# Performance work log

Hardware: AMD Instinct MI355X
Metric: run time of the kernel (lower is better)

The kernel has to match this reference:

```python
import jax, jax.numpy as jnp
import numpy as np

N_NODES = 100000      # total nodes across batch (50 graphs x 2000 nodes)
N_EDGES = 1600000     # avg degree 16
D = 64                # input_dim = hidden dims = output_dim
L = 3                 # number of GIN layers actually executed
NUM_GRAPHS = 50
NODES_PER_GRAPH = 2000
CAT_D = L * D         # 192, concat of hidden layer outputs


def setup_inputs() -> dict:
    key = jax.random.key(0)
    ks = jax.random.split(key, 12)
    s = 1.0 / np.sqrt(D)          # torch Linear init scale
    s2 = 1.0 / np.sqrt(CAT_D)
    return {
        "x": jax.random.normal(ks[0], (N_NODES, D), jnp.float32),
        "edge_index": jax.random.randint(ks[1], (2, N_EDGES), 0, N_NODES),
        "edge_weight": jax.random.uniform(ks[2], (N_EDGES,), jnp.float32),
        "batch": jnp.repeat(jnp.arange(NUM_GRAPHS), NODES_PER_GRAPH),  # sorted graph ids
        "W1": jax.random.uniform(ks[3], (L, D, D), jnp.float32, -s, s),
        "b1": jax.random.uniform(ks[4], (L, D), jnp.float32, -s, s),
        "W2": jax.random.uniform(ks[5], (L, D, D), jnp.float32, -s, s),
        "b2": jax.random.uniform(ks[6], (L, D), jnp.float32, -s, s),
        "eps": jnp.zeros((L,), jnp.float32),  # train_eps init 0.0
        "lin_w": jax.random.uniform(ks[7], (CAT_D, D), jnp.float32, -s2, s2),
        "lin_b": jax.random.uniform(ks[8], (D,), jnp.float32, -s2, s2),
    }


def reference(x, edge_index, edge_weight, batch, W1, b1, W2, b2, eps, lin_w, lin_b):
    src, dst = edge_index[0], edge_index[1]
    ew = edge_weight[:, None]
    h = x
    hiddens = []
    for l in range(L):
        # weighted GIN: aggregate sum_j w_ij * h_j at destination nodes
        agg = jax.ops.segment_sum(h[src] * ew, dst, num_segments=N_NODES)
        z = (1.0 + eps[l]) * h + agg
        # GIN MLP: Linear -> LeakyReLU -> Linear
        z = jax.nn.leaky_relu(z @ W1[l] + b1[l]) @ W2[l] + b2[l]
        hiddens.append(z)              # hiddens store pre-activation conv output
        h = jax.nn.leaky_relu(z)       # activation feeds next layer (dropout=0)
    h_cat = jnp.concatenate(hiddens, axis=-1)          # [N, 192]
    pooled = jax.ops.segment_sum(h_cat, batch, num_segments=NUM_GRAPHS)  # global_add_pool
    return pooled @ lin_w + lin_b                      # [NUM_GRAPHS, D]
```

## Files before the change

### kernel.cpp

```cpp
#include <hip/hip_runtime.h>

#define N_NODES 100000
#define N_EDGES 1600000
#define DD 64
#define NLAYER 3
#define NUM_GRAPHS 50
#define NODES_PER_GRAPH 2000
#define CAT_D (NLAYER * DD)
#define MROWS 80
#define MLP_THREADS 320
#define LPITCH 72

#define NPB 256
#define NB ((N_NODES + NPB - 1) / NPB)
#define BPAD 6144
#define ECHUNK 4096

#define GNODES 32
#define WECAP 288

typedef __attribute__((ext_vector_type(8))) short short8;
typedef __attribute__((ext_vector_type(4))) float float4v;

__device__ __forceinline__ float bf2f(unsigned short u) {
    return __uint_as_float(((unsigned)u) << 16);
}
__device__ __forceinline__ unsigned short f2bf(float f) {
    unsigned u = __float_as_uint(f);
    unsigned r = u + 0x7FFF + ((u >> 16) & 1);
    return (unsigned short)(r >> 16);
}
__device__ __forceinline__ float bflo(unsigned u) {
    return __uint_as_float(u << 16);
}
__device__ __forceinline__ float bfhi(unsigned u) {
    return __uint_as_float(u & 0xFFFF0000u);
}

__global__ __launch_bounds__(256) void convert_x_kernel(
    const float* __restrict__ x, unsigned short* __restrict__ hx)
{
    int i = (blockIdx.x * blockDim.x + threadIdx.x) * 4;
    if (i + 3 < N_NODES * DD) {
        float4 v = *(const float4*)&x[i];
        hx[i]     = f2bf(v.x);
        hx[i + 1] = f2bf(v.y);
        hx[i + 2] = f2bf(v.z);
        hx[i + 3] = f2bf(v.w);
    }
}

__global__ __launch_bounds__(256) void convert_w_kernel(
    const float* __restrict__ W1, const float* __restrict__ W2,
    unsigned short* __restrict__ W1t, unsigned short* __restrict__ W2t,
    int* __restrict__ cursor)
{
    int idx = blockIdx.x * blockDim.x + threadIdx.x;
    if (idx < NB) cursor[idx] = idx * BPAD;
    if (idx >= 2 * NLAYER * DD * DD) return;
    int which = idx / (NLAYER * DD * DD);
    int rem = idx % (NLAYER * DD * DD);
    int l = rem / (DD * DD);
    int t = rem % (DD * DD);
    int n = t >> 6, k = t & 63;
    const float* W = which ? W2 : W1;
    unsigned short* Wt = which ? W2t : W1t;
    Wt[l * DD * DD + n * DD + k] = f2bf(W[l * DD * DD + k * DD + n]);
}

__global__ __launch_bounds__(256) void bin_kernel(
    const int* __restrict__ src, const int* __restrict__ dst,
    const float* __restrict__ ew, int* __restrict__ cursor,
    uint2* __restrict__ binned)
{
    __shared__ uint2 stage[ECHUNK];
    __shared__ unsigned short bkt[ECHUNK];
    __shared__ int cnt[512];
    __shared__ int base[512];
    __shared__ int ssum[256];
    __shared__ int gbase[512];

    const int tid = threadIdx.x;
    const int start = blockIdx.x * ECHUNK;
    const int count = min(ECHUNK, N_EDGES - start);

    cnt[tid] = 0;
    cnt[tid + 256] = 0;
    __syncthreads();

    unsigned pk1[16], pk2[16];
    int eb[16], er[16];
    #pragma unroll
    for (int k = 0; k < 16; ++k) {
        int i = tid + k * 256;
        if (i < count) {
            int e = start + i;
            int s = src[e];
            int d = dst[e];
            float w = ew[e];
            int b = d >> 8;
            pk1[k] = (unsigned)s | ((unsigned)(d & 255) << 17);
            pk2[k] = __float_as_uint(w);
            eb[k] = b;
            er[k] = atomicAdd(&cnt[b], 1);
        } else {
            eb[k] = -1;
        }
    }
    __syncthreads();

    int c0 = cnt[2 * tid], c1 = cnt[2 * tid + 1];
    ssum[tid] = c0 + c1;
    __syncthreads();
    for (int off = 1; off < 256; off <<= 1) {
        int x = (tid >= off) ? ssum[tid - off] : 0;
        __syncthreads();
        ssum[tid] += x;
        __syncthreads();
    }
    int ex = (tid > 0) ? ssum[tid - 1] : 0;
    base[2 * tid] = ex;
    base[2 * tid + 1] = ex + c0;

    if (2 * tid < NB && c0 > 0)     gbase[2 * tid]     = atomicAdd(&cursor[2 * tid], c0);
    if (2 * tid + 1 < NB && c1 > 0) gbase[2 * tid + 1] = atomicAdd(&cursor[2 * tid + 1], c1);
    __syncthreads();

    #pragma unroll
    for (int k = 0; k < 16; ++k) {
        if (eb[k] >= 0) {
            int p = base[eb[k]] + er[k];
            stage[p].x = pk1[k];
            stage[p].y = pk2[k];
            bkt[p] = (unsigned short)eb[k];
        }
    }
    __syncthreads();

    for (int i = tid; i < count; i += 256) {
        int b = bkt[i];
        binned[gbase[b] + (i - base[b])] = stage[i];
    }
}

__global__ __launch_bounds__(256) void localsort_kernel(
    const int* __restrict__ cursor, const uint2* __restrict__ binned,
    uint2* __restrict__ s_edge, int* __restrict__ beg, int* __restrict__ end)
{
    __shared__ int deg[NPB];
    __shared__ int rb[NPB];
    __shared__ int cur[NPB];

    const int nb = blockIdx.x;
    const int tid = threadIdx.x;
    const int bstart = nb * BPAD;
    const int count = cursor[nb] - bstart;

    deg[tid] = 0;
    __syncthreads();
    for (int i = tid; i < count; i += 256) {
        unsigned w = binned[bstart + i].x;
        atomicAdd(&deg[(w >> 17) & 255], 1);
    }
    __syncthreads();

    int v = deg[tid];
    rb[tid] = v;
    __syncthreads();
    for (int off = 1; off < 256; off <<= 1) {
        int x = (tid >= off) ? rb[tid - off] : 0;
        __syncthreads();
        rb[tid] += x;
        __syncthreads();
    }
    int ex = rb[tid] - v;
    cur[tid] = ex;
    int node = nb * NPB + tid;
    if (node < N_NODES) {
        beg[node] = bstart + ex;
        end[node] = bstart + ex + v;
    }
    __syncthreads();

    for (int i = tid; i < count; i += 256) {
        uint2 e = binned[bstart + i];
        int d = (e.x >> 17) & 255;
        int r = atomicAdd(&cur[d], 1);
        uint2 o;
        o.x = e.x & 0x1FFFF;
        o.y = e.y;
        s_edge[bstart + r] = o;
    }
}

__global__ __launch_bounds__(256) void gather_kernel(
    const uint4* __restrict__ h4, const int* __restrict__ beg,
    const int* __restrict__ end, const uint2* __restrict__ s_edge,
    const float* __restrict__ eps, int l, uint4* __restrict__ z4)
{
    __shared__ uint2 eds[4 * WECAP];

    const int w    = threadIdx.x >> 6;
    const int lane = threadIdx.x & 63;
    const int o    = lane >> 3;
    const int fl   = lane & 7;
    const int nbase = blockIdx.x * GNODES + w * 8;
    const int node  = nbase + o;

    const int ebeg = beg[nbase];
    const int cnt  = end[nbase + 7] - ebeg;
    uint2* wl = &eds[w * WECAP];
    const bool lds_ok = (cnt <= WECAP);
    if (lds_ok) {
        for (int i = lane; i < cnt; i += 64) wl[i] = s_edge[ebeg + i];
    }

    const int gbeg = beg[node];
    const int deg  = end[node] - gbeg;

    float acc[4][8];
    #pragma unroll
    for (int c = 0; c < 4; ++c)
        #pragma unroll
        for (int j = 0; j < 8; ++j) acc[c][j] = 0.f;

    const uint4* hfl = h4 + fl;

    if (lds_ok) {
        const int bi = gbeg - ebeg;
        for (int it = 0; it < deg; it += 4) {
            #pragma unroll
            for (int c = 0; c < 4; ++c) {
                bool ok = (it + c) < deg;
                int idx = ok ? (bi + it + c) : bi;
                uint2 p = wl[idx];
                float wv = ok ? __uint_as_float(p.y) : 0.f;
                uint4 r = hfl[(long)p.x * 8];
                acc[c][0] += bflo(r.x) * wv;  acc[c][1] += bfhi(r.x) * wv;
                acc[c][2] += bflo(r.y) * wv;  acc[c][3] += bfhi(r.y) * wv;
                acc[c][4] += bflo(r.z) * wv;  acc[c][5] += bfhi(r.z) * wv;
                acc[c][6] += bflo(r.w) * wv;  acc[c][7] += bfhi(r.w) * wv;
            }
        }
    } else {
        for (int it = 0; it < deg; it += 4) {
            #pragma unroll
            for (int c = 0; c < 4; ++c) {
                bool ok = (it + c) < deg;
                int idx = ok ? (gbeg + it + c) : gbeg;
                uint2 p = s_edge[idx];
                float wv = ok ? __uint_as_float(p.y) : 0.f;
                uint4 r = hfl[(long)p.x * 8];
                acc[c][0] += bflo(r.x) * wv;  acc[c][1] += bfhi(r.x) * wv;
                acc[c][2] += bflo(r.y) * wv;  acc[c][3] += bfhi(r.y) * wv;
                acc[c][4] += bflo(r.z) * wv;  acc[c][5] += bfhi(r.z) * wv;
                acc[c][6] += bflo(r.w) * wv;  acc[c][7] += bfhi(r.w) * wv;
            }
        }
    }

    float s[8];
    #pragma unroll
    for (int j = 0; j < 8; ++j)
        s[j] = (acc[0][j] + acc[1][j]) + (acc[2][j] + acc[3][j]);

    const float e1 = 1.0f + eps[l];
    uint4 selfr = hfl[(long)node * 8];
    float z0 = e1 * bflo(selfr.x) + s[0];
    float z1 = e1 * bfhi(selfr.x) + s[1];
    float z2 = e1 * bflo(selfr.y) + s[2];
    float z3 = e1 * bfhi(selfr.y) + s[3];
    float z4v = e1 * bflo(selfr.z) + s[4];
    float z5 = e1 * bfhi(selfr.z) + s[5];
    float z6 = e1 * bflo(selfr.w) + s[6];
    float z7 = e1 * bfhi(selfr.w) + s[7];
    uint4 ov;
    ov.x = (unsigned)f2bf(z0) | ((unsigned)f2bf(z1) << 16);
    ov.y = (unsigned)f2bf(z2) | ((unsigned)f2bf(z3) << 16);
    ov.z = (unsigned)f2bf(z4v) | ((unsigned)f2bf(z5) << 16);
    ov.w = (unsigned)f2bf(z6) | ((unsigned)f2bf(z7) << 16);
    z4[(long)node * 8 + fl] = ov;
}

__global__ __launch_bounds__(MLP_THREADS) void mlp_kernel(
    const unsigned short* __restrict__ z_in,
    const unsigned short* __restrict__ W1t, const unsigned short* __restrict__ W2t,
    const float* __restrict__ b1l, const float* __restrict__ b2l,
    int l, unsigned short* __restrict__ h_out, float* __restrict__ pooled)
{
    __shared__ __align__(16) unsigned short zs[MROWS * LPITCH];
    __shared__ __align__(16) unsigned short w1s[DD * LPITCH];
    __shared__ __align__(16) unsigned short w2s[DD * LPITCH];
    __shared__ float red[5 * DD];

    const int tid  = threadIdx.x;
    const int lane = tid & 63;
    const int w    = tid >> 6;
    const int m15  = lane & 15;
    const int quad = lane >> 4;
    const long base = (long)blockIdx.x * MROWS;

    for (int idx = tid; idx < MROWS * 8; idx += MLP_THREADS) {
        int row = idx >> 3, seg = idx & 7;
        *(int4*)&zs[row * LPITCH + seg * 8] =
            *(const int4*)&z_in[(base + row) * DD + seg * 8];
    }
    for (int idx = tid; idx < DD * 8; idx += MLP_THREADS) {
        int row = idx >> 3, seg = idx & 7;
        *(int4*)&w1s[row * LPITCH + seg * 8] =
            *(const int4*)&W1t[(size_t)l * DD * DD + row * DD + seg * 8];
        *(int4*)&w2s[row * LPITCH + seg * 8] =
            *(const int4*)&W2t[(size_t)l * DD * DD + row * DD + seg * 8];
    }
    __syncthreads();

    {
        short8 a0 = *(const short8*)&zs[(w * 16 + m15) * LPITCH + quad * 8];
        short8 a1 = *(const short8*)&zs[(w * 16 + m15) * LPITCH + 32 + quad * 8];
        #pragma unroll
        for (int n = 0; n < 4; ++n) {
            short8 b0 = *(const short8*)&w1s[(n * 16 + m15) * LPITCH + quad * 8];
            short8 b1 = *(const short8*)&w1s[(n * 16 + m15) * LPITCH + 32 + quad * 8];
            float4v acc = {0.f, 0.f, 0.f, 0.f};
            acc = __builtin_amdgcn_mfma_f32_16x16x32_bf16(a0, b0, acc, 0, 0, 0);
            acc = __builtin_amdgcn_mfma_f32_16x16x32_bf16(a1, b1, acc, 0, 0, 0);
            int col = n * 16 + m15;
            float bv = b1l[col];
            #pragma unroll
            for (int r = 0; r < 4; ++r) {
                int row = w * 16 + quad * 4 + r;
                float t = acc[r] + bv;
                t = t > 0.0f ? t : 0.01f * t;
                zs[row * LPITCH + col] = f2bf(t);
            }
        }
    }

    float psum[4];
    {
        short8 a0 = *(const short8*)&zs[(w * 16 + m15) * LPITCH + quad * 8];
        short8 a1 = *(const short8*)&zs[(w * 16 + m15) * LPITCH + 32 + quad * 8];
        #pragma unroll
        for (int n = 0; n < 4; ++n) {
            short8 b0 = *(const short8*)&w2s[(n * 16 + m15) * LPITCH + quad * 8];
            short8 b1 = *(const short8*)&w2s[(n * 16 + m15) * LPITCH + 32 + quad * 8];
            float4v acc = {0.f, 0.f, 0.f, 0.f};
            acc = __builtin_amdgcn_mfma_f32_16x16x32_bf16(a0, b0, acc, 0, 0, 0);
            acc = __builtin_amdgcn_mfma_f32_16x16x32_bf16(a1, b1, acc, 0, 0, 0);
            int col = n * 16 + m15;
            float bv = b2l[col];
            float ps = 0.0f;
            #pragma unroll
            for (int r = 0; r < 4; ++r) {
                int row = w * 16 + quad * 4 + r;
                float z2 = acc[r] + bv;
                ps += z2;
                float hv = z2 > 0.0f ? z2 : 0.01f * z2;
                zs[row * LPITCH + col] = f2bf(hv);
            }
            psum[n] = ps;
        }
    }
    #pragma unroll
    for (int n = 0; n < 4; ++n) {
        float v = psum[n];
        v += __shfl_xor(v, 16);
        v += __shfl_xor(v, 32);
        if (quad == 0) red[w * DD + n * 16 + m15] = v;
    }
    __syncthreads();

    for (int idx = tid; idx < MROWS * 8; idx += MLP_THREADS) {
        int row = idx >> 3, seg = idx & 7;
        *(int4*)&h_out[(base + row) * DD + seg * 8] =
            *(const int4*)&zs[row * LPITCH + seg * 8];
    }
    if (tid < DD) {
        float tot = red[tid] + red[DD + tid] + red[2 * DD + tid]
                  + red[3 * DD + tid] + red[4 * DD + tid];
        int g = blockIdx.x / (NODES_PER_GRAPH / MROWS);
        atomicAdd(&pooled[g * CAT_D + l * DD + tid], tot);
    }
}

__global__ __launch_bounds__(64) void final_kernel(
    const float* __restrict__ pooled, const float* __restrict__ lin_w,
    const float* __restrict__ lin_b, float* __restrict__ out)
{
    int g = blockIdx.x;
    int j = threadIdx.x;
    float acc = lin_b[j];
    for (int k = 0; k < CAT_D; ++k)
        acc += pooled[g * CAT_D + k] * lin_w[k * DD + j];
    out[g * DD + j] = acc;
}

extern "C" void kernel_launch(void* const* d_in, const int* in_sizes, int n_in,
                              void* d_out, int out_size, void* d_ws, size_t ws_size,
                              hipStream_t stream)
{
    const float* x     = (const float*)d_in[0];
    const int*   ei    = (const int*)d_in[1];
    const float* ew    = (const float*)d_in[2];
    const float* W1    = (const float*)d_in[4];
    const float* b1    = (const float*)d_in[5];
    const float* W2    = (const float*)d_in[6];
    const float* b2    = (const float*)d_in[7];
    const float* eps   = (const float*)d_in[8];
    const float* lin_w = (const float*)d_in[9];
    const float* lin_b = (const float*)d_in[10];
    float* out = (float*)d_out;

    const int* src = ei;
    const int* dst = ei + N_EDGES;

    char* wsb = (char*)d_ws;
    size_t off = 0;
    auto alloc = [&](size_t bytes) -> void* {
        off = (off + 15) & ~(size_t)15;
        void* p = wsb + off;
        off += bytes;
        return p;
    };
    unsigned short* hX   = (unsigned short*)alloc((size_t)N_NODES * DD * 2);
    unsigned short* hA   = (unsigned short*)alloc((size_t)N_NODES * DD * 2);
    unsigned short* zbuf = (unsigned short*)alloc((size_t)N_NODES * DD * 2);
    unsigned short* W1t  = (unsigned short*)alloc((size_t)NLAYER * DD * DD * 2);
    unsigned short* W2t  = (unsigned short*)alloc((size_t)NLAYER * DD * DD * 2);
    float* pooled        = (float*)alloc((size_t)NUM_GRAPHS * CAT_D * 4);
    int*   cursor        = (int*)alloc((size_t)NB * 4);
    int*   beg           = (int*)alloc((size_t)N_NODES * 4);
    int*   end_          = (int*)alloc((size_t)N_NODES * 4);
    uint2* binned        = (uint2*)alloc((size_t)NB * BPAD * 8);
    uint2* s_edge        = (uint2*)alloc((size_t)NB * BPAD * 8);

    convert_x_kernel<<<(N_NODES * DD / 4 + 255) / 256, 256, 0, stream>>>(x, hX);
    convert_w_kernel<<<(2 * NLAYER * DD * DD + 255) / 256, 256, 0, stream>>>(
        W1, W2, W1t, W2t, cursor);

    bin_kernel<<<(N_EDGES + ECHUNK - 1) / ECHUNK, 256, 0, stream>>>(
        src, dst, ew, cursor, binned);
    localsort_kernel<<<NB, 256, 0, stream>>>(cursor, binned, s_edge, beg, end_);

    hipMemsetAsync(pooled, 0, NUM_GRAPHS * CAT_D * sizeof(float), stream);

    const unsigned short* h_cur = hX;
    unsigned short* h_nexts[3] = { hA, hX, hA };
    for (int l = 0; l < NLAYER; ++l) {
        gather_kernel<<<N_NODES / GNODES, 256, 0, stream>>>(
            (const uint4*)h_cur, beg, end_, s_edge, eps, l,
            (uint4*)zbuf);

        unsigned short* h_next = h_nexts[l];
        mlp_kernel<<<N_NODES / MROWS, MLP_THREADS, 0, stream>>>(
            zbuf, W1t, W2t,
            b1 + (size_t)l * DD, b2 + (size_t)l * DD,
            l, h_next, pooled);
        h_cur = h_next;
    }

    final_kernel<<<NUM_GRAPHS, 64, 0, stream>>>(pooled, lin_w, lin_b, out);
}
```

Before: 280.0 us.

## Fuse neighbor gather into MLP kernel and skip final layer hidden write

```diff
diff --git a/kernel.cpp b/kernel.cpp
--- a/kernel.cpp
+++ b/kernel.cpp
@@ -16,15 +16,11 @@
 #define BPAD 6144
 #define ECHUNK 4096
 
-#define GNODES 32
 #define WECAP 288
 
 typedef __attribute__((ext_vector_type(8))) short short8;
 typedef __attribute__((ext_vector_type(4))) float float4v;
 
-__device__ __forceinline__ float bf2f(unsigned short u) {
-    return __uint_as_float(((unsigned)u) << 16);
-}
 __device__ __forceinline__ unsigned short f2bf(float f) {
     unsigned u = __float_as_uint(f);
     unsigned r = u + 0x7FFF + ((u >> 16) & 1);
@@ -193,118 +189,25 @@
     }
 }
 
-__global__ __launch_bounds__(256) void gather_kernel(
+__global__ __launch_bounds__(MLP_THREADS) void layer_kernel(
     const uint4* __restrict__ h4, const int* __restrict__ beg,
     const int* __restrict__ end, const uint2* __restrict__ s_edge,
-    const float* __restrict__ eps, int l, uint4* __restrict__ z4)
-{
-    __shared__ uint2 eds[4 * WECAP];
-
-    const int w    = threadIdx.x >> 6;
-    const int lane = threadIdx.x & 63;
-    const int o    = lane >> 3;
-    const int fl   = lane & 7;
-    const int nbase = blockIdx.x * GNODES + w * 8;
-    const int node  = nbase + o;
-
-    const int ebeg = beg[nbase];
-    const int cnt  = end[nbase + 7] - ebeg;
-    uint2* wl = &eds[w * WECAP];
-    const bool lds_ok = (cnt <= WECAP);
-    if (lds_ok) {
-        for (int i = lane; i < cnt; i += 64) wl[i] = s_edge[ebeg + i];
-    }
-
-    const int gbeg = beg[node];
-    const int deg  = end[node] - gbeg;
-
-    float acc[4][8];
-    #pragma unroll
-    for (int c = 0; c < 4; ++c)
-        #pragma unroll
-        for (int j = 0; j < 8; ++j) acc[c][j] = 0.f;
-
-    const uint4* hfl = h4 + fl;
-
-    if (lds_ok) {
-        const int bi = gbeg - ebeg;
-        for (int it = 0; it < deg; it += 4) {
-            #pragma unroll
-            for (int c = 0; c < 4; ++c) {
-                bool ok = (it + c) < deg;
-                int idx = ok ? (bi + it + c) : bi;
-                uint2 p = wl[idx];
-                float wv = ok ? __uint_as_float(p.y) : 0.f;
-                uint4 r = hfl[(long)p.x * 8];
-                acc[c][0] += bflo(r.x) * wv;  acc[c][1] += bfhi(r.x) * wv;
-                acc[c][2] += bflo(r.y) * wv;  acc[c][3] += bfhi(r.y) * wv;
-                acc[c][4] += bflo(r.z) * wv;  acc[c][5] += bfhi(r.z) * wv;
-                acc[c][6] += bflo(r.w) * wv;  acc[c][7] += bfhi(r.w) * wv;
-            }
-        }
-    } else {
-        for (int it = 0; it < deg; it += 4) {
-            #pragma unroll
-            for (int c = 0; c < 4; ++c) {
-                bool ok = (it + c) < deg;
-                int idx = ok ? (gbeg + it + c) : gbeg;
-                uint2 p = s_edge[idx];
-                float wv = ok ? __uint_as_float(p.y) : 0.f;
-                uint4 r = hfl[(long)p.x * 8];
-                acc[c][0] += bflo(r.x) * wv;  acc[c][1] += bfhi(r.x) * wv;
-                acc[c][2] += bflo(r.y) * wv;  acc[c][3] += bfhi(r.y) * wv;
-                acc[c][4] += bflo(r.z) * wv;  acc[c][5] += bfhi(r.z) * wv;
-                acc[c][6] += bflo(r.w) * wv;  acc[c][7] += bfhi(r.w) * wv;
-            }
-        }
-    }
-
-    float s[8];
-    #pragma unroll
-    for (int j = 0; j < 8; ++j)
-        s[j] = (acc[0][j] + acc[1][j]) + (acc[2][j] + acc[3][j]);
-
-    const float e1 = 1.0f + eps[l];
-    uint4 selfr = hfl[(long)node * 8];
-    float z0 = e1 * bflo(selfr.x) + s[0];
-    float z1 = e1 * bfhi(selfr.x) + s[1];
-    float z2 = e1 * bflo(selfr.y) + s[2];
-    float z3 = e1 * bfhi(selfr.y) + s[3];
-    float z4v = e1 * bflo(selfr.z) + s[4];
-    float z5 = e1 * bfhi(selfr.z) + s[5];
-    float z6 = e1 * bflo(selfr.w) + s[6];
-    float z7 = e1 * bfhi(selfr.w) + s[7];
-    uint4 ov;
-    ov.x = (unsigned)f2bf(z0) | ((unsigned)f2bf(z1) << 16);
-    ov.y = (unsigned)f2bf(z2) | ((unsigned)f2bf(z3) << 16);
-    ov.z = (unsigned)f2bf(z4v) | ((unsigned)f2bf(z5) << 16);
-    ov.w = (unsigned)f2bf(z6) | ((unsigned)f2bf(z7) << 16);
-    z4[(long)node * 8 + fl] = ov;
-}
-
-__global__ __launch_bounds__(MLP_THREADS) void mlp_kernel(
-    const unsigned short* __restrict__ z_in,
+    const float* __restrict__ eps, int l,
     const unsigned short* __restrict__ W1t, const unsigned short* __restrict__ W2t,
     const float* __restrict__ b1l, const float* __restrict__ b2l,
-    int l, unsigned short* __restrict__ h_out, float* __restrict__ pooled)
+    unsigned short* __restrict__ h_out, float* __restrict__ pooled)
 {
     __shared__ __align__(16) unsigned short zs[MROWS * LPITCH];
     __shared__ __align__(16) unsigned short w1s[DD * LPITCH];
     __shared__ __align__(16) unsigned short w2s[DD * LPITCH];
+    __shared__ uint2 eds[5 * WECAP];
     __shared__ float red[5 * DD];
 
     const int tid  = threadIdx.x;
     const int lane = tid & 63;
     const int w    = tid >> 6;
-    const int m15  = lane & 15;
-    const int quad = lane >> 4;
     const long base = (long)blockIdx.x * MROWS;
 
-    for (int idx = tid; idx < MROWS * 8; idx += MLP_THREADS) {
-        int row = idx >> 3, seg = idx & 7;
-        *(int4*)&zs[row * LPITCH + seg * 8] =
-            *(const int4*)&z_in[(base + row) * DD + seg * 8];
-    }
     for (int idx = tid; idx < DD * 8; idx += MLP_THREADS) {
         int row = idx >> 3, seg = idx & 7;
         *(int4*)&w1s[row * LPITCH + seg * 8] =
@@ -312,7 +215,89 @@
         *(int4*)&w2s[row * LPITCH + seg * 8] =
             *(const int4*)&W2t[(size_t)l * DD * DD + row * DD + seg * 8];
     }
-    __syncthreads();
+
+    const int o  = lane >> 3;
+    const int fl = lane & 7;
+    const float e1 = 1.0f + eps[l];
+    const uint4* hfl = h4 + fl;
+    uint2* wl = &eds[w * WECAP];
+
+    for (int r = 0; r < 2; ++r) {
+        const int nbase = (int)base + w * 16 + r * 8;
+        const int node  = nbase + o;
+        const int ebeg = beg[nbase];
+        const int cnt  = end[nbase + 7] - ebeg;
+        const bool lds_ok = (cnt <= WECAP);
+        if (lds_ok) {
+            for (int i = lane; i < cnt; i += 64) wl[i] = s_edge[ebeg + i];
+        }
+        const int gbeg = beg[node];
+        const int deg  = end[node] - gbeg;
+
+        float acc[4][8];
+        #pragma unroll
+        for (int c = 0; c < 4; ++c)
+            #pragma unroll
+            for (int j = 0; j < 8; ++j) acc[c][j] = 0.f;
+
+        if (lds_ok) {
+            const int bi = gbeg - ebeg;
+            for (int it = 0; it < deg; it += 4) {
+                #pragma unroll
+                for (int c = 0; c < 4; ++c) {
+                    bool ok = (it + c) < deg;
+                    int idx = ok ? (bi + it + c) : bi;
+                    uint2 p = wl[idx];
+                    float wv = ok ? __uint_as_float(p.y) : 0.f;
+                    uint4 rr = hfl[(long)p.x * 8];
+                    acc[c][0] += bflo(rr.x) * wv;  acc[c][1] += bfhi(rr.x) * wv;
+                    acc[c][2] += bflo(rr.y) * wv;  acc[c][3] += bfhi(rr.y) * wv;
+                    acc[c][4] += bflo(rr.z) * wv;  acc[c][5] += bfhi(rr.z) * wv;
+                    acc[c][6] += bflo(rr.w) * wv;  acc[c][7] += bfhi(rr.w) * wv;
+                }
+            }
+        } else {
+            for (int it = 0; it < deg; it += 4) {
+                #pragma unroll
+                for (int c = 0; c < 4; ++c) {
+                    bool ok = (it + c) < deg;
+                    int idx = ok ? (gbeg + it + c) : gbeg;
+                    uint2 p = s_edge[idx];
+                    float wv = ok ? __uint_as_float(p.y) : 0.f;
+                    uint4 rr = hfl[(long)p.x * 8];
+                    acc[c][0] += bflo(rr.x) * wv;  acc[c][1] += bfhi(rr.x) * wv;
+                    acc[c][2] += bflo(rr.y) * wv;  acc[c][3] += bfhi(rr.y) * wv;
+                    acc[c][4] += bflo(rr.z) * wv;  acc[c][5] += bfhi(rr.z) * wv;
+                    acc[c][6] += bflo(rr.w) * wv;  acc[c][7] += bfhi(rr.w) * wv;
+                }
+            }
+        }
+
+        float s[8];
+        #pragma unroll
+        for (int j = 0; j < 8; ++j)
+            s[j] = (acc[0][j] + acc[1][j]) + (acc[2][j] + acc[3][j]);
+
+        uint4 selfr = hfl[(long)node * 8];
+        float z0 = e1 * bflo(selfr.x) + s[0];
+        float z1 = e1 * bfhi(selfr.x) + s[1];
+        float z2v = e1 * bflo(selfr.y) + s[2];
+        float z3 = e1 * bfhi(selfr.y) + s[3];
+        float z4v = e1 * bflo(selfr.z) + s[4];
+        float z5 = e1 * bfhi(selfr.z) + s[5];
+        float z6 = e1 * bflo(selfr.w) + s[6];
+        float z7 = e1 * bfhi(selfr.w) + s[7];
+        uint4 ov;
+        ov.x = (unsigned)f2bf(z0) | ((unsigned)f2bf(z1) << 16);
+        ov.y = (unsigned)f2bf(z2v) | ((unsigned)f2bf(z3) << 16);
+        ov.z = (unsigned)f2bf(z4v) | ((unsigned)f2bf(z5) << 16);
+        ov.w = (unsigned)f2bf(z6) | ((unsigned)f2bf(z7) << 16);
+        *(uint4*)&zs[(w * 16 + r * 8 + o) * LPITCH + fl * 8] = ov;
+    }
+    __syncthreads();
+
+    const int m15  = lane & 15;
+    const int quad = lane >> 4;
 
     {
         short8 a0 = *(const short8*)&zs[(w * 16 + m15) * LPITCH + quad * 8];
@@ -370,10 +355,12 @@
     }
     __syncthreads();
 
-    for (int idx = tid; idx < MROWS * 8; idx += MLP_THREADS) {
-        int row = idx >> 3, seg = idx & 7;
-        *(int4*)&h_out[(base + row) * DD + seg * 8] =
-            *(const int4*)&zs[row * LPITCH + seg * 8];
+    if (h_out) {
+        for (int idx = tid; idx < MROWS * 8; idx += MLP_THREADS) {
+            int row = idx >> 3, seg = idx & 7;
+            *(int4*)&h_out[(base + row) * DD + seg * 8] =
+                *(const int4*)&zs[row * LPITCH + seg * 8];
+        }
     }
     if (tid < DD) {
         float tot = red[tid] + red[DD + tid] + red[2 * DD + tid]
@@ -424,7 +411,6 @@
     };
     unsigned short* hX   = (unsigned short*)alloc((size_t)N_NODES * DD * 2);
     unsigned short* hA   = (unsigned short*)alloc((size_t)N_NODES * DD * 2);
-    unsigned short* zbuf = (unsigned short*)alloc((size_t)N_NODES * DD * 2);
     unsigned short* W1t  = (unsigned short*)alloc((size_t)NLAYER * DD * DD * 2);
     unsigned short* W2t  = (unsigned short*)alloc((size_t)NLAYER * DD * DD * 2);
     float* pooled        = (float*)alloc((size_t)NUM_GRAPHS * CAT_D * 4);
@@ -444,19 +430,13 @@
 
     hipMemsetAsync(pooled, 0, NUM_GRAPHS * CAT_D * sizeof(float), stream);
 
-    const unsigned short* h_cur = hX;
-    unsigned short* h_nexts[3] = { hA, hX, hA };
+    const unsigned short* h_ins[3]  = { hX, hA, hX };
+    unsigned short*       h_outs[3] = { hA, hX, nullptr };
     for (int l = 0; l < NLAYER; ++l) {
-        gather_kernel<<<N_NODES / GNODES, 256, 0, stream>>>(
-            (const uint4*)h_cur, beg, end_, s_edge, eps, l,
-            (uint4*)zbuf);
-
-        unsigned short* h_next = h_nexts[l];
-        mlp_kernel<<<N_NODES / MROWS, MLP_THREADS, 0, stream>>>(
-            zbuf, W1t, W2t,
-            b1 + (size_t)l * DD, b2 + (size_t)l * DD,
-            l, h_next, pooled);
-        h_cur = h_next;
+        layer_kernel<<<N_NODES / MROWS, MLP_THREADS, 0, stream>>>(
+            (const uint4*)h_ins[l], beg, end_, s_edge, eps, l,
+            W1t, W2t, b1 + (size_t)l * DD, b2 + (size_t)l * DD,
+            h_outs[l], pooled);
     }
 
     final_kernel<<<NUM_GRAPHS, 64, 0, stream>>>(pooled, lin_w, lin_b, out);
```

Result: slower. 290.4 us (+3.7%).
